# Kernel optimization log

Measured on AMD Instinct MI355X. Metric: run time of the kernel, lower is better.

The kernel has to match this reference:

```python
import jax, jax.numpy as jnp
import numpy as np
from jax import lax

B, T, D = 8, 4096, 512
UNITS = 512
WINDOW = 2


def setup_inputs() -> dict:
    key = jax.random.key(0)
    k1, k2, k3 = jax.random.split(key, 3)
    x = jax.random.normal(k1, (B, T, D), dtype=jnp.float32)
    # keras kernel shape is (window, 1, input_dim, 3*units); drop the dummy height dim
    kernel = jax.random.uniform(k2, (WINDOW, D, 3 * UNITS), dtype=jnp.float32,
                                minval=-0.05, maxval=0.05)
    bias = jnp.zeros((3 * UNITS,), dtype=jnp.float32)
    return {"x": x, "kernel": kernel, "bias": bias}


def reference(x, kernel, bias):
    window, d_in, u3 = kernel.shape
    units = u3 // 3
    # causal padding: window-1 zeros on the left of the time axis
    xp = jnp.pad(x, ((0, 0), (window - 1, 0), (0, 0)))
    # 1D valid conv -> gates [B, T, 3*units]
    gates = lax.conv_general_dilated(
        xp, kernel, window_strides=(1,), padding='VALID',
        dimension_numbers=('NWC', 'WIO', 'NWC')) + bias
    z = jnp.tanh(gates[..., :units])
    f = jax.nn.sigmoid(gates[..., units:2 * units])
    o = jax.nn.sigmoid(gates[..., 2 * units:])

    # fo-pool recurrence: c_t = f_t * c_{t-1} + (1 - f_t) * z_t ; out_t = o_t * c_t
    def step(c, zfo):
        z_t, f_t, o_t = zfo
        c = f_t * c + (1.0 - f_t) * z_t
        return c, o_t * c

    c0 = jnp.zeros((x.shape[0], units), dtype=x.dtype)
    zT = jnp.swapaxes(z, 0, 1)  # [T, B, U]
    fT = jnp.swapaxes(f, 0, 1)
    oT = jnp.swapaxes(o, 0, 1)
    _, ysT = lax.scan(step, c0, (zT, fT, oT))
    return jnp.swapaxes(ysT, 0, 1)  # [B, T, U] (return_sequences=True)
```

## Files before the change

kernel.cpp:

```cpp
#include <hip/hip_runtime.h>
#include <cstdint>
#include <cstddef>

#define BB   8
#define TT   4096
#define DD   512
#define UU   512
#define NN   1536
#define KK   1024
#define MM   32768
#define NCH  128
#define CHL  32

using bf16x8 = __attribute__((ext_vector_type(8))) __bf16;
using f32x4  = __attribute__((ext_vector_type(4))) float;

__device__ __forceinline__ unsigned short f2bf(float f) {
    unsigned u = __float_as_uint(f);
    u += 0x7fffu + ((u >> 16) & 1u);
    return (unsigned short)(u >> 16);
}
__device__ __forceinline__ float bf2f(unsigned short s) {
    return __uint_as_float(((unsigned)s) << 16);
}
__device__ __forceinline__ float sigf(float x) { return 1.0f / (1.0f + __expf(-x)); }
__device__ __forceinline__ float tanh_(float x) { return 1.0f - 2.0f / (1.0f + __expf(2.0f * x)); }

__device__ __forceinline__ void async16(const void* g, void* l) {
    __builtin_amdgcn_global_load_lds(
        (__attribute__((address_space(1))) void*)g,
        (__attribute__((address_space(3))) void*)l, 16, 0, 0);
}

__global__ void k_pad(const float* __restrict__ x, unsigned short* __restrict__ xpad) {
    int b = blockIdx.y;
    int q = blockIdx.x * blockDim.x + threadIdx.x;
    if (q >= 4097 * 128) return;
    int tp = q >> 7;
    int d  = (q & 127) << 2;
    size_t oi = ((size_t)b * 4097 + tp) * 512 + d;
    ushort4 o;
    if (tp == 0) {
        o.x = o.y = o.z = o.w = 0;
    } else {
        float4 v = *(const float4*)(x + ((size_t)b * 4096 + (tp - 1)) * 512 + d);
        o.x = f2bf(v.x); o.y = f2bf(v.y); o.z = f2bf(v.z); o.w = f2bf(v.w);
    }
    *(ushort4*)(xpad + oi) = o;
}

__global__ void k_tr(const float* __restrict__ kern, unsigned short* __restrict__ kT) {
    __shared__ float tile[32][33];
    int k0 = blockIdx.x * 32;
    int n0 = blockIdx.y * 32;
    int c  = threadIdx.x & 31;
    int r0 = threadIdx.x >> 5;
#pragma unroll
    for (int rr = r0; rr < 32; rr += 8)
        tile[rr][c] = kern[(size_t)(k0 + rr) * NN + n0 + c];
    __syncthreads();
#pragma unroll
    for (int rr = r0; rr < 32; rr += 8)
        kT[(size_t)(n0 + rr) * KK + k0 + c] = f2bf(tile[c][rr]);
}

__global__ __launch_bounds__(256) void k_gemm(
    const unsigned short* __restrict__ xpad,
    const unsigned short* __restrict__ kT,
    const float* __restrict__ bias,
    unsigned short* __restrict__ gates)
{
    __shared__ unsigned short As[128 * 64];
    __shared__ unsigned short Bs[128 * 64];
    const int tid  = threadIdx.x;
    const int m0   = blockIdx.x * 128;
    const int n0   = blockIdx.y * 128;
    const int boff = m0 >> 12;
    const size_t abase = (size_t)(m0 + boff) * 512;

    f32x4 acc[4][4] = {};

    const int wid  = tid >> 6;
    const int lane = tid & 63;
    const int wm   = (wid & 1) * 64;
    const int wn   = (wid >> 1) * 64;
    const int lrow = lane & 15;
    const int quad = lane >> 4;

    for (int kk = 0; kk < KK; kk += 64) {
#pragma unroll
        for (int q = 0; q < 4; ++q) {
            int L   = q * 256 + tid;
            int row = L >> 3;
            int sp  = L & 7;
            int sl  = sp ^ (row & 7);
            async16(xpad + abase + (size_t)row * 512 + kk + sl * 8, As + (size_t)L * 8);
            async16(kT + (size_t)(n0 + row) * KK + kk + sl * 8, Bs + (size_t)L * 8);
        }
        __syncthreads();
#pragma unroll
        for (int ks = 0; ks < 2; ++ks) {
            bf16x8 af[4], bfr[4];
#pragma unroll
            for (int i = 0; i < 4; ++i) {
                int row = wm + i * 16 + lrow;
                int sp  = (ks * 4 + quad) ^ (row & 7);
                af[i] = *(const bf16x8*)(As + row * 64 + sp * 8);
            }
#pragma unroll
            for (int j = 0; j < 4; ++j) {
                int row = wn + j * 16 + lrow;
                int sp  = (ks * 4 + quad) ^ (row & 7);
                bfr[j] = *(const bf16x8*)(Bs + row * 64 + sp * 8);
            }
#pragma unroll
            for (int i = 0; i < 4; ++i)
#pragma unroll
                for (int j = 0; j < 4; ++j)
                    acc[i][j] = __builtin_amdgcn_mfma_f32_16x16x32_bf16(af[i], bfr[j], acc[i][j], 0, 0, 0);
        }
        __syncthreads();
    }

#pragma unroll
    for (int j = 0; j < 4; ++j) {
        int col  = n0 + wn + j * 16 + lrow;
        float bv = bias[col];
#pragma unroll
        for (int i = 0; i < 4; ++i) {
            int rbase = m0 + wm + i * 16 + quad * 4;
#pragma unroll
            for (int r = 0; r < 4; ++r) {
                gates[(size_t)(rbase + r) * NN + col] = f2bf(acc[i][j][r] + bv);
            }
        }
    }
}

__global__ void k_scanA(const unsigned short* __restrict__ gates,
                        float* __restrict__ Fp, float* __restrict__ Ce) {
    int chunk = blockIdx.x;
    int b     = blockIdx.y;
    int u     = threadIdx.x << 2;
    float c0 = 0, c1 = 0, c2 = 0, c3 = 0;
    float F0 = 1, F1 = 1, F2 = 1, F3 = 1;
    size_t g = ((size_t)b * TT + (size_t)chunk * CHL) * NN + u;
#pragma unroll 4
    for (int i = 0; i < CHL; ++i) {
        ushort4 gz = *(const ushort4*)(gates + g);
        ushort4 gf = *(const ushort4*)(gates + g + UU);
        g += NN;
        float f0 = sigf(bf2f(gf.x)), z0 = tanh_(bf2f(gz.x));
        float f1 = sigf(bf2f(gf.y)), z1 = tanh_(bf2f(gz.y));
        float f2 = sigf(bf2f(gf.z)), z2 = tanh_(bf2f(gz.z));
        float f3 = sigf(bf2f(gf.w)), z3 = tanh_(bf2f(gz.w));
        c0 = f0 * c0 + (1.0f - f0) * z0; F0 *= f0;
        c1 = f1 * c1 + (1.0f - f1) * z1; F1 *= f1;
        c2 = f2 * c2 + (1.0f - f2) * z2; F2 *= f2;
        c3 = f3 * c3 + (1.0f - f3) * z3; F3 *= f3;
    }
    size_t ci = ((size_t)b * NCH + chunk) * UU + u;
    *(float4*)(Fp + ci) = make_float4(F0, F1, F2, F3);
    *(float4*)(Ce + ci) = make_float4(c0, c1, c2, c3);
}

__global__ void k_scanB(const float* __restrict__ Fp, const float* __restrict__ Ce,
                        float* __restrict__ Cin) {
    int b = blockIdx.x;
    int u = threadIdx.x << 2;
    float4 c = make_float4(0, 0, 0, 0);
    for (int k = 0; k < NCH; ++k) {
        size_t idx = ((size_t)b * NCH + k) * UU + u;
        *(float4*)(Cin + idx) = c;
        float4 F = *(const float4*)(Fp + idx);
        float4 E = *(const float4*)(Ce + idx);
        c.x = F.x * c.x + E.x;
        c.y = F.y * c.y + E.y;
        c.z = F.z * c.z + E.z;
        c.w = F.w * c.w + E.w;
    }
}

__global__ void k_scanC(const unsigned short* __restrict__ gates,
                        const float* __restrict__ Cin, float* __restrict__ out) {
    int chunk = blockIdx.x;
    int b     = blockIdx.y;
    int u     = threadIdx.x << 2;
    size_t ci = ((size_t)b * NCH + chunk) * UU + u;
    float4 cv = *(const float4*)(Cin + ci);
    float c0 = cv.x, c1 = cv.y, c2 = cv.z, c3 = cv.w;
    size_t g = ((size_t)b * TT + (size_t)chunk * CHL) * NN + u;
    size_t o = ((size_t)b * TT + (size_t)chunk * CHL) * UU + u;
#pragma unroll 4
    for (int i = 0; i < CHL; ++i) {
        ushort4 gz = *(const ushort4*)(gates + g);
        ushort4 gf = *(const ushort4*)(gates + g + UU);
        ushort4 go = *(const ushort4*)(gates + g + 2 * UU);
        g += NN;
        float f0 = sigf(bf2f(gf.x)), z0 = tanh_(bf2f(gz.x)), o0 = sigf(bf2f(go.x));
        float f1 = sigf(bf2f(gf.y)), z1 = tanh_(bf2f(gz.y)), o1 = sigf(bf2f(go.y));
        float f2 = sigf(bf2f(gf.z)), z2 = tanh_(bf2f(gz.z)), o2 = sigf(bf2f(go.z));
        float f3 = sigf(bf2f(gf.w)), z3 = tanh_(bf2f(gz.w)), o3 = sigf(bf2f(go.w));
        c0 = f0 * c0 + (1.0f - f0) * z0;
        c1 = f1 * c1 + (1.0f - f1) * z1;
        c2 = f2 * c2 + (1.0f - f2) * z2;
        c3 = f3 * c3 + (1.0f - f3) * z3;
        *(float4*)(out + o) = make_float4(o0 * c0, o1 * c1, o2 * c2, o3 * c3);
        o += UU;
    }
}

extern "C" void kernel_launch(void* const* d_in, const int* in_sizes, int n_in,
                              void* d_out, int out_size, void* d_ws, size_t ws_size,
                              hipStream_t stream) {
    const float* x    = (const float*)d_in[0];
    const float* kern = (const float*)d_in[1];
    const float* bias = (const float*)d_in[2];
    float* out = (float*)d_out;
    char* ws = (char*)d_ws;

    unsigned short* xpad  = (unsigned short*)(ws + 0);
    unsigned short* kT    = (unsigned short*)(ws + 33562624);
    unsigned short* gates = (unsigned short*)(ws + 36708352);
    float* Fp  = (float*)(ws + 137371648);
    float* Ce  = (float*)(ws + 139468800);
    float* Cin = (float*)(ws + 141565952);

    hipLaunchKernelGGL(k_pad,   dim3(2049, 8), dim3(256), 0, stream, x, xpad);
    hipLaunchKernelGGL(k_tr,    dim3(32, 48),  dim3(256), 0, stream, kern, kT);
    hipLaunchKernelGGL(k_gemm,  dim3(256, 12), dim3(256), 0, stream, xpad, kT, bias, gates);
    hipLaunchKernelGGL(k_scanA, dim3(128, 8),  dim3(128), 0, stream, gates, Fp, Ce);
    hipLaunchKernelGGL(k_scanB, dim3(8),       dim3(128), 0, stream, Fp, Ce, Cin);
    hipLaunchKernelGGL(k_scanC, dim3(128, 8),  dim3(128), 0, stream, gates, Cin, out);
}
```

Baseline: 328.2 us.

## Merge prep kernels, remap GEMM tiles per XCD, fuse scan phases cooperatively

Merges the pad and kernel-transpose launches into one prep kernel. Remaps the GEMM's 1D grid so consecutive blocks on the same XCD share M tiles, which should improve L2 reuse. Replaces the three scan kernels with one cooperative kernel that uses grid.sync between phases, and parallelises the middle carry pass across 4096 threads instead of 8 blocks. This cuts launch overhead and gives the serial carry pass more parallelism, at the cost of two grid-wide barriers and the need for all blocks to be co-resident.

```diff
diff --git a/kernel.cpp b/kernel.cpp
--- a/kernel.cpp
+++ b/kernel.cpp
@@ -1,6 +1,9 @@
 #include <hip/hip_runtime.h>
+#include <hip/hip_cooperative_groups.h>
 #include <cstdint>
 #include <cstddef>
+
+namespace cg = cooperative_groups;
 
 #define BB   8
 #define TT   4096
@@ -32,36 +35,44 @@
         (__attribute__((address_space(3))) void*)l, 16, 0, 0);
 }
 
-__global__ void k_pad(const float* __restrict__ x, unsigned short* __restrict__ xpad) {
-    int b = blockIdx.y;
-    int q = blockIdx.x * blockDim.x + threadIdx.x;
-    if (q >= 4097 * 128) return;
-    int tp = q >> 7;
-    int d  = (q & 127) << 2;
-    size_t oi = ((size_t)b * 4097 + tp) * 512 + d;
-    ushort4 o;
-    if (tp == 0) {
-        o.x = o.y = o.z = o.w = 0;
+__global__ void k_prep(const float* __restrict__ x, unsigned short* __restrict__ xpad,
+                       const float* __restrict__ kern, unsigned short* __restrict__ kT) {
+    int bx = blockIdx.x;
+    int by = blockIdx.y;
+    int tid = threadIdx.x;
+    if (bx < 2049) {
+        int q = bx * 256 + tid;
+        if (q >= 4097 * 128) return;
+        int tp = q >> 7;
+        int d  = (q & 127) << 2;
+        size_t oi = ((size_t)by * 4097 + tp) * 512 + d;
+        ushort4 o;
+        if (tp == 0) {
+            o.x = o.y = o.z = o.w = 0;
+        } else {
+            float4 v = *(const float4*)(x + ((size_t)by * 4096 + (tp - 1)) * 512 + d);
+            o.x = f2bf(v.x); o.y = f2bf(v.y); o.z = f2bf(v.z); o.w = f2bf(v.w);
+        }
+        *(ushort4*)(xpad + oi) = o;
     } else {
-        float4 v = *(const float4*)(x + ((size_t)b * 4096 + (tp - 1)) * 512 + d);
-        o.x = f2bf(v.x); o.y = f2bf(v.y); o.z = f2bf(v.z); o.w = f2bf(v.w);
-    }
-    *(ushort4*)(xpad + oi) = o;
-}
-
-__global__ void k_tr(const float* __restrict__ kern, unsigned short* __restrict__ kT) {
-    __shared__ float tile[32][33];
-    int k0 = blockIdx.x * 32;
-    int n0 = blockIdx.y * 32;
-    int c  = threadIdx.x & 31;
-    int r0 = threadIdx.x >> 5;
-#pragma unroll
-    for (int rr = r0; rr < 32; rr += 8)
-        tile[rr][c] = kern[(size_t)(k0 + rr) * NN + n0 + c];
-    __syncthreads();
-#pragma unroll
-    for (int rr = r0; rr < 32; rr += 8)
-        kT[(size_t)(n0 + rr) * KK + k0 + c] = f2bf(tile[c][rr]);
+        __shared__ float tile[32][33];
+        int idx = (bx - 2049) * 8 + by;
+        int c  = tid & 31;
+        int r0 = tid >> 5;
+        for (int t8 = 0; t8 < 8; ++t8) {
+            int tnum = idx * 8 + t8;
+            int k0 = (tnum & 31) * 32;
+            int n0 = (tnum >> 5) * 32;
+#pragma unroll
+            for (int rr = r0; rr < 32; rr += 8)
+                tile[rr][c] = kern[(size_t)(k0 + rr) * NN + n0 + c];
+            __syncthreads();
+#pragma unroll
+            for (int rr = r0; rr < 32; rr += 8)
+                kT[(size_t)(n0 + rr) * KK + k0 + c] = f2bf(tile[c][rr]);
+            __syncthreads();
+        }
+    }
 }
 
 __global__ __launch_bounds__(256) void k_gemm(
@@ -73,8 +84,13 @@
     __shared__ unsigned short As[128 * 64];
     __shared__ unsigned short Bs[128 * 64];
     const int tid  = threadIdx.x;
-    const int m0   = blockIdx.x * 128;
-    const int n0   = blockIdx.y * 128;
+    const int bi   = blockIdx.x;
+    const int xcd  = bi & 7;
+    const int loc  = bi >> 3;
+    const int mt   = xcd * 32 + loc / 12;
+    const int nt   = loc % 12;
+    const int m0   = mt * 128;
+    const int n0   = nt * 128;
     const int boff = m0 >> 12;
     const size_t abase = (size_t)(m0 + boff) * 512;
 
@@ -137,76 +153,91 @@
     }
 }
 
-__global__ void k_scanA(const unsigned short* __restrict__ gates,
-                        float* __restrict__ Fp, float* __restrict__ Ce) {
-    int chunk = blockIdx.x;
-    int b     = blockIdx.y;
-    int u     = threadIdx.x << 2;
-    float c0 = 0, c1 = 0, c2 = 0, c3 = 0;
-    float F0 = 1, F1 = 1, F2 = 1, F3 = 1;
-    size_t g = ((size_t)b * TT + (size_t)chunk * CHL) * NN + u;
+__global__ __launch_bounds__(128) void k_scan(
+    const unsigned short* __restrict__ gates,
+    float* __restrict__ Fp, float* __restrict__ Ce, float* __restrict__ Cin,
+    float* __restrict__ out)
+{
+    cg::grid_group grid = cg::this_grid();
+    const int bid   = blockIdx.x;
+    const int chunk = bid & 127;
+    const int b     = bid >> 7;
+    const int u     = threadIdx.x << 2;
+
+    {
+        float c0 = 0, c1 = 0, c2 = 0, c3 = 0;
+        float F0 = 1, F1 = 1, F2 = 1, F3 = 1;
+        size_t g = ((size_t)b * TT + (size_t)chunk * CHL) * NN + u;
 #pragma unroll 4
-    for (int i = 0; i < CHL; ++i) {
-        ushort4 gz = *(const ushort4*)(gates + g);
-        ushort4 gf = *(const ushort4*)(gates + g + UU);
-        g += NN;
-        float f0 = sigf(bf2f(gf.x)), z0 = tanh_(bf2f(gz.x));
-        float f1 = sigf(bf2f(gf.y)), z1 = tanh_(bf2f(gz.y));
-        float f2 = sigf(bf2f(gf.z)), z2 = tanh_(bf2f(gz.z));
-        float f3 = sigf(bf2f(gf.w)), z3 = tanh_(bf2f(gz.w));
-        c0 = f0 * c0 + (1.0f - f0) * z0; F0 *= f0;
-        c1 = f1 * c1 + (1.0f - f1) * z1; F1 *= f1;
-        c2 = f2 * c2 + (1.0f - f2) * z2; F2 *= f2;
-        c3 = f3 * c3 + (1.0f - f3) * z3; F3 *= f3;
-    }
-    size_t ci = ((size_t)b * NCH + chunk) * UU + u;
-    *(float4*)(Fp + ci) = make_float4(F0, F1, F2, F3);
-    *(float4*)(Ce + ci) = make_float4(c0, c1, c2, c3);
-}
-
-__global__ void k_scanB(const float* __restrict__ Fp, const float* __restrict__ Ce,
-                        float* __restrict__ Cin) {
-    int b = blockIdx.x;
-    int u = threadIdx.x << 2;
-    float4 c = make_float4(0, 0, 0, 0);
-    for (int k = 0; k < NCH; ++k) {
-        size_t idx = ((size_t)b * NCH + k) * UU + u;
-        *(float4*)(Cin + idx) = c;
-        float4 F = *(const float4*)(Fp + idx);
-        float4 E = *(const float4*)(Ce + idx);
-        c.x = F.x * c.x + E.x;
-        c.y = F.y * c.y + E.y;
-        c.z = F.z * c.z + E.z;
-        c.w = F.w * c.w + E.w;
-    }
-}
-
-__global__ void k_scanC(const unsigned short* __restrict__ gates,
-                        const float* __restrict__ Cin, float* __restrict__ out) {
-    int chunk = blockIdx.x;
-    int b     = blockIdx.y;
-    int u     = threadIdx.x << 2;
-    size_t ci = ((size_t)b * NCH + chunk) * UU + u;
-    float4 cv = *(const float4*)(Cin + ci);
-    float c0 = cv.x, c1 = cv.y, c2 = cv.z, c3 = cv.w;
-    size_t g = ((size_t)b * TT + (size_t)chunk * CHL) * NN + u;
-    size_t o = ((size_t)b * TT + (size_t)chunk * CHL) * UU + u;
+        for (int i = 0; i < CHL; ++i) {
+            ushort4 gz = *(const ushort4*)(gates + g);
+            ushort4 gf = *(const ushort4*)(gates + g + UU);
+            g += NN;
+            float f0 = sigf(bf2f(gf.x)), z0 = tanh_(bf2f(gz.x));
+            float f1 = sigf(bf2f(gf.y)), z1 = tanh_(bf2f(gz.y));
+            float f2 = sigf(bf2f(gf.z)), z2 = tanh_(bf2f(gz.z));
+            float f3 = sigf(bf2f(gf.w)), z3 = tanh_(bf2f(gz.w));
+            c0 = f0 * c0 + (1.0f - f0) * z0; F0 *= f0;
+            c1 = f1 * c1 + (1.0f - f1) * z1; F1 *= f1;
+            c2 = f2 * c2 + (1.0f - f2) * z2; F2 *= f2;
+            c3 = f3 * c3 + (1.0f - f3) * z3; F3 *= f3;
+        }
+        size_t ci = ((size_t)b * NCH + chunk) * UU + u;
+        *(float4*)(Fp + ci) = make_float4(F0, F1, F2, F3);
+        *(float4*)(Ce + ci) = make_float4(c0, c1, c2, c3);
+    }
+    __threadfence();
+    grid.sync();
+
+    {
+        int gid = bid * 128 + threadIdx.x;
+        if (gid < BB * UU) {
+            int bb = gid >> 9;
+            int uu = gid & 511;
+            size_t base = (size_t)bb * NCH * UU + uu;
+            float c = 0.0f;
+#pragma unroll
+            for (int k0 = 0; k0 < NCH; k0 += 8) {
+                float F[8], E[8];
+#pragma unroll
+                for (int j = 0; j < 8; ++j) {
+                    F[j] = Fp[base + (size_t)(k0 + j) * UU];
+                    E[j] = Ce[base + (size_t)(k0 + j) * UU];
+                }
+#pragma unroll
+                for (int j = 0; j < 8; ++j) {
+                    Cin[base + (size_t)(k0 + j) * UU] = c;
+                    c = F[j] * c + E[j];
+                }
+            }
+        }
+    }
+    __threadfence();
+    grid.sync();
+
+    {
+        size_t ci = ((size_t)b * NCH + chunk) * UU + u;
+        float4 cv = *(const float4*)(Cin + ci);
+        float c0 = cv.x, c1 = cv.y, c2 = cv.z, c3 = cv.w;
+        size_t g = ((size_t)b * TT + (size_t)chunk * CHL) * NN + u;
+        size_t o = ((size_t)b * TT + (size_t)chunk * CHL) * UU + u;
 #pragma unroll 4
-    for (int i = 0; i < CHL; ++i) {
-        ushort4 gz = *(const ushort4*)(gates + g);
-        ushort4 gf = *(const ushort4*)(gates + g + UU);
-        ushort4 go = *(const ushort4*)(gates + g + 2 * UU);
-        g += NN;
-        float f0 = sigf(bf2f(gf.x)), z0 = tanh_(bf2f(gz.x)), o0 = sigf(bf2f(go.x));
-        float f1 = sigf(bf2f(gf.y)), z1 = tanh_(bf2f(gz.y)), o1 = sigf(bf2f(go.y));
-        float f2 = sigf(bf2f(gf.z)), z2 = tanh_(bf2f(gz.z)), o2 = sigf(bf2f(go.z));
-        float f3 = sigf(bf2f(gf.w)), z3 = tanh_(bf2f(gz.w)), o3 = sigf(bf2f(go.w));
-        c0 = f0 * c0 + (1.0f - f0) * z0;
-        c1 = f1 * c1 + (1.0f - f1) * z1;
-        c2 = f2 * c2 + (1.0f - f2) * z2;
-        c3 = f3 * c3 + (1.0f - f3) * z3;
-        *(float4*)(out + o) = make_float4(o0 * c0, o1 * c1, o2 * c2, o3 * c3);
-        o += UU;
+        for (int i = 0; i < CHL; ++i) {
+            ushort4 gz = *(const ushort4*)(gates + g);
+            ushort4 gf = *(const ushort4*)(gates + g + UU);
+            ushort4 go = *(const ushort4*)(gates + g + 2 * UU);
+            g += NN;
+            float f0 = sigf(bf2f(gf.x)), z0 = tanh_(bf2f(gz.x)), o0 = sigf(bf2f(go.x));
+            float f1 = sigf(bf2f(gf.y)), z1 = tanh_(bf2f(gz.y)), o1 = sigf(bf2f(go.y));
+            float f2 = sigf(bf2f(gf.z)), z2 = tanh_(bf2f(gz.z)), o2 = sigf(bf2f(go.z));
+            float f3 = sigf(bf2f(gf.w)), z3 = tanh_(bf2f(gz.w)), o3 = sigf(bf2f(go.w));
+            c0 = f0 * c0 + (1.0f - f0) * z0;
+            c1 = f1 * c1 + (1.0f - f1) * z1;
+            c2 = f2 * c2 + (1.0f - f2) * z2;
+            c3 = f3 * c3 + (1.0f - f3) * z3;
+            *(float4*)(out + o) = make_float4(o0 * c0, o1 * c1, o2 * c2, o3 * c3);
+            o += UU;
+        }
     }
 }
 
@@ -226,10 +257,9 @@
     float* Ce  = (float*)(ws + 139468800);
     float* Cin = (float*)(ws + 141565952);
 
-    hipLaunchKernelGGL(k_pad,   dim3(2049, 8), dim3(256), 0, stream, x, xpad);
-    hipLaunchKernelGGL(k_tr,    dim3(32, 48),  dim3(256), 0, stream, kern, kT);
-    hipLaunchKernelGGL(k_gemm,  dim3(256, 12), dim3(256), 0, stream, xpad, kT, bias, gates);
-    hipLaunchKernelGGL(k_scanA, dim3(128, 8),  dim3(128), 0, stream, gates, Fp, Ce);
-    hipLaunchKernelGGL(k_scanB, dim3(8),       dim3(128), 0, stream, Fp, Ce, Cin);
-    hipLaunchKernelGGL(k_scanC, dim3(128, 8),  dim3(128), 0, stream, gates, Cin, out);
-}
+    hipLaunchKernelGGL(k_prep, dim3(2049 + 24, 8), dim3(256), 0, stream, x, xpad, kern, kT);
+    hipLaunchKernelGGL(k_gemm, dim3(3072), dim3(256), 0, stream, xpad, kT, bias, gates);
+
+    void* args[] = { (void*)&gates, (void*)&Fp, (void*)&Ce, (void*)&Cin, (void*)&out };
+    hipLaunchCooperativeKernel((void*)k_scan, dim3(1024), dim3(128), args, 0, stream);
+}
```

New measurement: 652.6 us. 1.99x slower.
